# Optimization experiments

Measured on AMD Instinct MI355X. Metric: run time of the kernel, lower is better.

## Reference

```python
import jax, jax.numpy as jnp
import numpy as np

B, S, D, H, DFF = 2, 2048, 512, 8, 2048
DK = D // H
EPS = 1e-6  # LayerNormalization eps


def _ln(x, a, b):
    # torch: alpha * (x - mean) / (std + eps) + bias, std is unbiased (ddof=1)
    m = jnp.mean(x, axis=-1, keepdims=True)
    s = jnp.std(x, axis=-1, keepdims=True, ddof=1)
    return a * (x - m) / (s + EPS) + b


def _mha(Q, K, V, mask, Wq, bq, Wk, bk, Wv, bv, Wo, bo):
    Bq, Sq = Q.shape[0], Q.shape[1]
    Sk = K.shape[1]
    q = (Q @ Wq + bq).reshape(Bq, Sq, H, DK).transpose(0, 2, 1, 3)  # bhqd
    k = (K @ Wk + bk).reshape(Bq, Sk, H, DK).transpose(0, 2, 1, 3)  # bhkd
    v = (V @ Wv + bv).reshape(Bq, Sk, H, DK).transpose(0, 2, 1, 3)  # bhkd
    scores = jnp.einsum('bhqd,bhkd->bhqk', q, k) / jnp.sqrt(jnp.float32(DK))
    scores = jnp.where(mask == 0, -jnp.inf, scores)  # masked_fill(mask==0, -inf)
    attn = jax.nn.softmax(scores, axis=-1)  # dropout is identity in eval
    out = jnp.einsum('bhqk,bhkd->bhqd', attn, v)
    out = out.transpose(0, 2, 1, 3).reshape(Bq, Sq, D)
    return out @ Wo + bo


def setup_inputs() -> dict:
    key = jax.random.key(0)
    ks = jax.random.split(key, 20)
    sc = 0.02
    inp = {
        'x': jax.random.normal(ks[0], (B, S, D), jnp.float32),
        'encoder_output': jax.random.normal(ks[1], (B, S, D), jnp.float32),
        'encoder_output_mask': jnp.broadcast_to(jnp.ones((S, S), jnp.int32), (B, 1, S, S)),
        'decoder_mask': jnp.broadcast_to(jnp.tril(jnp.ones((S, S), jnp.int32)), (B, 1, S, S)),
        'sa_Wq': jax.random.normal(ks[2], (D, D), jnp.float32) * sc,
        'sa_bq': jnp.zeros((D,), jnp.float32),
        'sa_Wk': jax.random.normal(ks[3], (D, D), jnp.float32) * sc,
        'sa_bk': jnp.zeros((D,), jnp.float32),
        'sa_Wv': jax.random.normal(ks[4], (D, D), jnp.float32) * sc,
        'sa_bv': jnp.zeros((D,), jnp.float32),
        'sa_Wo': jax.random.normal(ks[5], (D, D), jnp.float32) * sc,
        'sa_bo': jnp.zeros((D,), jnp.float32),
        'ca_Wq': jax.random.normal(ks[6], (D, D), jnp.float32) * sc,
        'ca_bq': jnp.zeros((D,), jnp.float32),
        'ca_Wk': jax.random.normal(ks[7], (D, D), jnp.float32) * sc,
        'ca_bk': jnp.zeros((D,), jnp.float32),
        'ca_Wv': jax.random.normal(ks[8], (D, D), jnp.float32) * sc,
        'ca_bv': jnp.zeros((D,), jnp.float32),
        'ca_Wo': jax.random.normal(ks[9], (D, D), jnp.float32) * sc,
        'ca_bo': jnp.zeros((D,), jnp.float32),
        'ff_W1': jax.random.normal(ks[10], (D, DFF), jnp.float32) * sc,
        'ff_b1': jnp.zeros((DFF,), jnp.float32),
        'ff_W2': jax.random.normal(ks[11], (DFF, D), jnp.float32) * sc,
        'ff_b2': jnp.zeros((D,), jnp.float32),
        'ln0_a': jnp.ones((1,), jnp.float32), 'ln0_b': jnp.zeros((1,), jnp.float32),
        'ln1_a': jnp.ones((1,), jnp.float32), 'ln1_b': jnp.zeros((1,), jnp.float32),
        'ln2_a': jnp.ones((1,), jnp.float32), 'ln2_b': jnp.zeros((1,), jnp.float32),
    }
    return inp


def reference(x, encoder_output, encoder_output_mask, decoder_mask,
              sa_Wq, sa_bq, sa_Wk, sa_bk, sa_Wv, sa_bv, sa_Wo, sa_bo,
              ca_Wq, ca_bq, ca_Wk, ca_bk, ca_Wv, ca_bv, ca_Wo, ca_bo,
              ff_W1, ff_b1, ff_W2, ff_b2,
              ln0_a, ln0_b, ln1_a, ln1_b, ln2_a, ln2_b):
    # Residual 0: pre-norm self-attention (dropout = identity in eval)
    n = _ln(x, ln0_a, ln0_b)
    x = x + _mha(n, n, n, decoder_mask, sa_Wq, sa_bq, sa_Wk, sa_bk, sa_Wv, sa_bv, sa_Wo, sa_bo)
    # Residual 1: pre-norm cross-attention
    n = _ln(x, ln1_a, ln1_b)
    x = x + _mha(n, encoder_output, encoder_output, encoder_output_mask,
                 ca_Wq, ca_bq, ca_Wk, ca_bk, ca_Wv, ca_bv, ca_Wo, ca_bo)
    # Residual 2: pre-norm FFN (Linear -> ReLU -> Linear)
    n = _ln(x, ln2_a, ln2_b)
    x = x + (jax.nn.relu(n @ ff_W1 + ff_b1) @ ff_W2 + ff_b2)
    return x
```

## Files before the change

### kernel.cpp

```cpp
#include <hip/hip_runtime.h>
#include <hip/hip_bf16.h>

typedef __bf16 bf16_t;
typedef __bf16 bf16x8_t __attribute__((ext_vector_type(8)));
typedef float f32x4_t __attribute__((ext_vector_type(4)));

static constexpr int B_ = 2, S_ = 2048, D_ = 512, H_ = 8, DK_ = 64, DFF_ = 2048;
static constexpr int M_ = B_ * S_;
static constexpr float QSCALE = 0.125f * 1.44269504f;

__device__ __forceinline__ unsigned pkbf(float a, float b) {
  union { bf16_t h; unsigned short u; } x, y;
  x.h = (bf16_t)a; y.h = (bf16_t)b;
  return (unsigned)x.u | ((unsigned)y.u << 16);
}

__device__ __forceinline__ void async16(bf16_t* lds, const bf16_t* g) {
  __builtin_amdgcn_global_load_lds((__attribute__((address_space(1))) void*)g,
                                   (__attribute__((address_space(3))) void*)lds,
                                   16, 0, 0);
}

struct PrepArg {
  const float* W[10]; bf16_t* T[10];
  const float* enc; bf16_t* encb;
  const float* x; bf16_t* xb; float2* stats0;
  float* stats12;
  float* csum[7];
};

__global__ __launch_bounds__(256) void prep(PrepArg a) {
  __shared__ float T[64 * 65];
  const int bx = blockIdx.x, tid = threadIdx.x;
  if (bx < 1024) {
    const float* W; bf16_t* Wt; int K, N, k0, n0;
    if (bx < 512) { int wi = bx >> 6, t = bx & 63; W = a.W[wi]; Wt = a.T[wi]; K = 512; N = 512; k0 = (t >> 3) * 64; n0 = (t & 7) * 64; }
    else if (bx < 768) { int t = bx - 512; W = a.W[8]; Wt = a.T[8]; K = 512; N = 2048; k0 = (t & 7) * 64; n0 = (t >> 3) * 64; }
    else { int t = bx - 768; W = a.W[9]; Wt = a.T[9]; K = 2048; N = 512; k0 = (t & 31) * 64; n0 = (t >> 5) * 64; }
#pragma unroll
    for (int p = 0; p < 4; ++p) {
      int e = p * 1024 + tid * 4;
      int kr = e >> 6, nc = e & 63;
      float4 f = *(const float4*)(W + (long)(k0 + kr) * N + n0 + nc);
      T[kr * 65 + nc + 0] = f.x; T[kr * 65 + nc + 1] = f.y;
      T[kr * 65 + nc + 2] = f.z; T[kr * 65 + nc + 3] = f.w;
    }
    __syncthreads();
#pragma unroll
    for (int p = 0; p < 4; ++p) {
      int e = p * 1024 + tid * 4;
      int nr = e >> 6, kc = e & 63;
      alignas(8) bf16_t t4[4];
#pragma unroll
      for (int j = 0; j < 4; ++j) t4[j] = (bf16_t)T[(kc + j) * 65 + nr];
      *(uint2*)(Wt + (long)(n0 + nr) * K + k0 + kc) = *(uint2*)t4;
    }
  } else if (bx < 2048) {
    const long i = ((long)(bx - 1024) * 256 + tid) * 8;
    float4 u = *(const float4*)(a.enc + i);
    float4 v = *(const float4*)(a.enc + i + 4);
    alignas(16) bf16_t t[8];
    t[0] = (bf16_t)u.x; t[1] = (bf16_t)u.y; t[2] = (bf16_t)u.z; t[3] = (bf16_t)u.w;
    t[4] = (bf16_t)v.x; t[5] = (bf16_t)v.y; t[6] = (bf16_t)v.z; t[7] = (bf16_t)v.w;
    *(uint4*)(a.encb + i) = *(uint4*)t;
  } else if (bx < 3072) {
    const int row = (bx - 2048) * 4 + (tid >> 6);
    const int lane = tid & 63;
    const float4* xr = (const float4*)(a.x + (long)row * D_);
    float4 v0 = xr[lane * 2], v1 = xr[lane * 2 + 1];
    float s = v0.x + v0.y + v0.z + v0.w + v1.x + v1.y + v1.z + v1.w;
    float ss = v0.x * v0.x + v0.y * v0.y + v0.z * v0.z + v0.w * v0.w +
               v1.x * v1.x + v1.y * v1.y + v1.z * v1.z + v1.w * v1.w;
#pragma unroll
    for (int m = 1; m < 64; m <<= 1) { s += __shfl_xor(s, m); ss += __shfl_xor(ss, m); }
    alignas(16) bf16_t y[8];
    y[0] = (bf16_t)v0.x; y[1] = (bf16_t)v0.y; y[2] = (bf16_t)v0.z; y[3] = (bf16_t)v0.w;
    y[4] = (bf16_t)v1.x; y[5] = (bf16_t)v1.y; y[6] = (bf16_t)v1.z; y[7] = (bf16_t)v1.w;
    ((uint4*)(a.xb + (long)row * D_))[lane] = *(uint4*)y;
    if (lane == 0) a.stats0[row] = make_float2(s, ss);
  } else if (bx < 3152) {
    __shared__ float red[256];
    int b3 = bx - 3072;
    const float* Wsrc; float* dst; int N, c0;
    if (b3 < 48) {
      const int map[6] = {0, 1, 2, 4, 5, 6};
      int wsel = b3 >> 3;
      Wsrc = a.W[map[wsel]]; dst = a.csum[wsel]; N = 512; c0 = (b3 & 7) * 64;
    } else { Wsrc = a.W[8]; dst = a.csum[6]; N = 2048; c0 = (b3 - 48) * 64; }
    const int col = c0 + (tid & 63);
    float p = 0.f;
    for (int k = tid >> 6; k < 512; k += 4) p += Wsrc[(long)k * N + col];
    red[tid] = p;
    __syncthreads();
    if (tid < 64) dst[c0 + tid] = red[tid] + red[tid + 64] + red[tid + 128] + red[tid + 192];
  } else {
    const int i = (bx - 3152) * 2048 + tid * 8;
    *(f32x4_t*)&a.stats12[i] = (f32x4_t){0.f, 0.f, 0.f, 0.f};
    *(f32x4_t*)&a.stats12[i + 4] = (f32x4_t){0.f, 0.f, 0.f, 0.f};
  }
}

__device__ __forceinline__ void ln_coef(float2 st, float ga, float gb,
                                        float& sc, float& sh) {
  const float mean = st.x * (1.0f / 512.0f);
  float var = (st.y - 512.0f * mean * mean) * (1.0f / 511.0f);
  var = fmaxf(var, 0.0f);
  sc = ga / (sqrtf(var) + 1e-6f);
  sh = gb - mean * sc;
}

struct G128 {
  const bf16_t* A[3]; const bf16_t* Wt[3];
  const float* bias[3]; const float* csum[3];
  void* out[3]; float osc[3];
  const float2* stats; const float* ga; const float* gb;
  int N; int zvt;
};

template <int RELU>
__global__ __launch_bounds__(256, 2) void gemm128(G128 a) {
  __shared__ bf16_t As[2][128 * 32];
  __shared__ bf16_t Bs[2][128 * 32];
  const int z = blockIdx.z;
  const bf16_t* A = a.A[z];
  const bf16_t* Wt = a.Wt[z];
  const float* bias = a.bias[z];
  const float* csum = a.csum[z];
  const int N = a.N;
  const int tid = threadIdx.x;
  const int wave = tid >> 6, lane = tid & 63, quad = lane >> 4, l15 = lane & 15;
  const long m0 = (long)blockIdx.x * 128;
  const long n0 = (long)blockIdx.y * 128;
  const int wm = (wave >> 1) * 64;
  const int wn = (wave & 1) * 64;

  const int r4 = lane >> 2;
  const int cg = (lane & 3) ^ ((lane >> 3) & 3);
  const bf16_t* Ab = A + m0 * 512 + cg * 8;
  const bf16_t* Bb = Wt + n0 * 512 + cg * 8;

  auto stage = [&](int buf, int k0) {
#pragma unroll
    for (int c = 0; c < 2; ++c) {
      const int row = wave * 32 + c * 16;
      async16(&As[buf][row * 32], Ab + (long)(row + r4) * 512 + k0);
      async16(&Bs[buf][row * 32], Bb + (long)(row + r4) * 512 + k0);
    }
  };

  f32x4_t acc[4][4];
#pragma unroll
  for (int i = 0; i < 4; ++i)
#pragma unroll
    for (int j = 0; j < 4; ++j) acc[i][j] = (f32x4_t){0.f, 0.f, 0.f, 0.f};

  const int sc8 = (quad ^ ((l15 >> 1) & 3)) * 8;
  stage(0, 0);
  for (int kt = 0; kt < 16; ++kt) {
    __syncthreads();
    if (kt + 1 < 16) stage((kt + 1) & 1, (kt + 1) * 32);
    const bf16_t* Al = &As[kt & 1][0];
    const bf16_t* Bl = &Bs[kt & 1][0];
    bf16x8_t af[4], bfr[4];
#pragma unroll
    for (int i = 0; i < 4; ++i) af[i] = *(const bf16x8_t*)&Al[(wm + i * 16 + l15) * 32 + sc8];
#pragma unroll
    for (int j = 0; j < 4; ++j) bfr[j] = *(const bf16x8_t*)&Bl[(wn + j * 16 + l15) * 32 + sc8];
#pragma unroll
    for (int i = 0; i < 4; ++i)
#pragma unroll
      for (int j = 0; j < 4; ++j)
        acc[i][j] = __builtin_amdgcn_mfma_f32_16x16x32_bf16(af[i], bfr[j], acc[i][j], 0, 0, 0);
  }

  const bool useln = (csum != nullptr);
  float scr[4][4], shr[4][4];
  if (useln) {
    const float gav = a.ga[0], gbv = a.gb[0];
#pragma unroll
    for (int i = 0; i < 4; ++i)
#pragma unroll
      for (int r = 0; r < 4; ++r) {
        const int row = (int)m0 + wm + i * 16 + quad * 4 + r;
        ln_coef(a.stats[row], gav, gbv, scr[i][r], shr[i][r]);
      }
  } else {
#pragma unroll
    for (int i = 0; i < 4; ++i)
#pragma unroll
      for (int r = 0; r < 4; ++r) { scr[i][r] = 1.f; shr[i][r] = 0.f; }
  }

  const bool isVt = (z == a.zvt);
  const float osc = a.osc[z];
#pragma unroll
  for (int i = 0; i < 4; ++i) {
#pragma unroll
    for (int j = 0; j < 4; ++j) {
      const int col = (int)n0 + wn + j * 16 + l15;
      const float cs = useln ? csum[col] : 0.f;
      const float bv = bias[col];
      float v[4];
#pragma unroll
      for (int r = 0; r < 4; ++r) {
        v[r] = scr[i][r] * acc[i][j][r] + shr[i][r] * cs + bv;
        if constexpr (RELU == 1) v[r] = fmaxf(v[r], 0.f);
      }
      if (isVt) {
        const int row0 = (int)m0 + wm + i * 16 + quad * 4;
        const int b = row0 >> 11, s = row0 & 2047;
        const long addr = ((long)(b * 8 + (col >> 6)) * 64 + (col & 63)) * 2048 + s;
        uint2 w;
        w.x = pkbf(v[0], v[1]);
        w.y = pkbf(v[2], v[3]);
        *(uint2*)((bf16_t*)a.out[z] + addr) = w;
      } else {
        bf16_t* outp = (bf16_t*)a.out[z];
#pragma unroll
        for (int r = 0; r < 4; ++r) {
          const long row = m0 + wm + i * 16 + quad * 4 + r;
          outp[row * N + col] = (bf16_t)(v[r] * osc);
        }
      }
    }
  }
}

template <bool STATS>
__global__ __launch_bounds__(256, 3) void gemm64(const bf16_t* __restrict__ A, int K,
                                                 const bf16_t* __restrict__ Wt,
                                                 const float* __restrict__ bias,
                                                 const float* __restrict__ res,
                                                 float* __restrict__ out,
                                                 bf16_t* __restrict__ outb,
                                                 float* __restrict__ statsOut) {
  __shared__ bf16_t As[2][64 * 64];
  __shared__ bf16_t Bs[2][128 * 64];
  const int tid = threadIdx.x;
  const int wave = tid >> 6, lane = tid & 63, quad = lane >> 4, l15 = lane & 15;
  const long m0 = (long)blockIdx.x * 64;
  const long n0 = (long)blockIdx.y * 128;
  const int wm = (wave >> 1) * 32;
  const int wn = (wave & 1) * 64;

  const int r8 = lane >> 3;
  const int cg = (lane & 7) ^ r8;
  const bf16_t* Ab = A + m0 * (long)K + cg * 8;
  const bf16_t* Bb = Wt + n0 * (long)K + cg * 8;

  auto stage = [&](int buf, int k0) {
#pragma unroll
    for (int c = 0; c < 2; ++c) {
      const int row = wave * 16 + c * 8;
      async16(&As[buf][row * 64], Ab + (long)(row + r8) * K + k0);
    }
#pragma unroll
    for (int c = 0; c < 4; ++c) {
      const int row = wave * 32 + c * 8;
      async16(&Bs[buf][row * 64], Bb + (long)(row + r8) * K + k0);
    }
  };

  f32x4_t acc[2][4];
#pragma unroll
  for (int i = 0; i < 2; ++i)
#pragma unroll
    for (int j = 0; j < 4; ++j) acc[i][j] = (f32x4_t){0.f, 0.f, 0.f, 0.f};

  const int KT = K >> 6;
  stage(0, 0);
  for (int kt = 0; kt < KT; ++kt) {
    __syncthreads();
    if (kt + 1 < KT) stage((kt + 1) & 1, (kt + 1) * 64);
    const bf16_t* Al = &As[kt & 1][0];
    const bf16_t* Bl = &Bs[kt & 1][0];
#pragma unroll
    for (int ks = 0; ks < 2; ++ks) {
      const int sc = ((ks * 4 + quad) ^ (l15 & 7)) * 8;
      bf16x8_t af[2], bfr[4];
#pragma unroll
      for (int i = 0; i < 2; ++i) af[i] = *(const bf16x8_t*)&Al[(wm + i * 16 + l15) * 64 + sc];
#pragma unroll
      for (int j = 0; j < 4; ++j) bfr[j] = *(const bf16x8_t*)&Bl[(wn + j * 16 + l15) * 64 + sc];
#pragma unroll
      for (int i = 0; i < 2; ++i)
#pragma unroll
        for (int j = 0; j < 4; ++j)
          acc[i][j] = __builtin_amdgcn_mfma_f32_16x16x32_bf16(af[i], bfr[j], acc[i][j], 0, 0, 0);
    }
  }

#pragma unroll
  for (int i = 0; i < 2; ++i) {
    float rs[4] = {0.f, 0.f, 0.f, 0.f}, rq[4] = {0.f, 0.f, 0.f, 0.f};
#pragma unroll
    for (int j = 0; j < 4; ++j) {
      const int col = (int)n0 + wn + j * 16 + l15;
      const float bv = bias[col];
#pragma unroll
      for (int r = 0; r < 4; ++r) {
        const long row = m0 + wm + i * 16 + quad * 4 + r;
        const float v = acc[i][j][r] + bv + res[row * 512 + col];
        out[row * 512 + col] = v;
        if constexpr (STATS) {
          outb[row * 512 + col] = (bf16_t)v;
          rs[r] += v;
          rq[r] += v * v;
        }
      }
    }
    if constexpr (STATS) {
#pragma unroll
      for (int r = 0; r < 4; ++r) {
#pragma unroll
        for (int m = 1; m < 16; m <<= 1) {
          rs[r] += __shfl_xor(rs[r], m);
          rq[r] += __shfl_xor(rq[r], m);
        }
        if (l15 == 0) {
          const long row = m0 + wm + i * 16 + quad * 4 + r;
          atomicAdd(&statsOut[row * 2], rs[r]);
          atomicAdd(&statsOut[row * 2 + 1], rq[r]);
        }
      }
    }
  }
}

template <bool CAUSAL>
__global__ __launch_bounds__(256, 3) void flash_attn(const bf16_t* __restrict__ Q,
                                                     const bf16_t* __restrict__ Kg,
                                                     const bf16_t* __restrict__ Vt,
                                                     float* __restrict__ po,
                                                     float* __restrict__ pl) {
  __shared__ bf16_t Ks[2][64 * 64];
  __shared__ bf16_t Vs[2][64 * 64];
  __shared__ bf16_t Ps[4][32 * 64];
  const int tid = threadIdx.x, wave = tid >> 6, lane = tid & 63;
  const int quad = lane >> 4, l15 = lane & 15;
  const int bh = blockIdx.y, b = bh >> 3, h = bh & 7;
  const int qt = CAUSAL ? (15 - (int)blockIdx.x) : (int)blockIdx.x;
  const int chunk = blockIdx.z;
  const int ntt = CAUSAL ? (2 * qt + 2) : 32;
  const int tstart = (chunk * ntt) / 3;
  const int tend = ((chunk + 1) * ntt) / 3;
  const int q0 = qt * 128;
  const long prow0 = ((long)(chunk * 16 + bh)) * 2048;

  if (tstart >= tend) {
    const long ob = (prow0 + q0) * 64;
#pragma unroll
    for (int p = 0; p < 8; ++p)
      *(f32x4_t*)&po[ob + (long)tid * 32 + p * 4] = (f32x4_t){0.f, 0.f, 0.f, 0.f};
    if (tid < 128) pl[prow0 + q0 + tid] = 0.f;
    return;
  }

  const int qw = q0 + wave * 32;
  const long base = (long)b * S_ * D_ + (long)h * DK_;
  const long vtbase = (long)bh * DK_ * S_;

  bf16x8_t qf[2][2];
#pragma unroll
  for (int qh = 0; qh < 2; ++qh)
#pragma unroll
    for (int ks = 0; ks < 2; ++ks)
      qf[qh][ks] = *(const bf16x8_t*)(Q + base + (long)(qw + qh * 16 + l15) * D_ + ks * 32 + quad * 8);

  const int r8 = lane >> 3;
  const int cg8 = (lane & 7) ^ r8;
  const bf16_t* Kb = Kg + base + cg8 * 8;
  const bf16_t* Vb = Vt + vtbase + cg8 * 8;

  auto stage = [&](int buf, int t) {
    const int kk0 = t * 64;
#pragma unroll
    for (int c = 0; c < 2; ++c) {
      const int row = wave * 16 + c * 8;
      async16(&Ks[buf][row * 64], Kb + (long)(kk0 + row + r8) * D_);
      async16(&Vs[buf][row * 64], Vb + (long)(row + r8) * S_ + kk0);
    }
  };

  float li[2] = {0.f, 0.f};
  f32x4_t o[2][4];
#pragma unroll
  for (int qh = 0; qh < 2; ++qh)
#pragma unroll
    for (int db = 0; db < 4; ++db) o[qh][db] = (f32x4_t){0.f, 0.f, 0.f, 0.f};

  bf16_t* Pw = &Ps[wave][0];
  const int pq7 = l15 & 7;

  stage(0, tstart);
  for (int t = tstart; t < tend; ++t) {
    const int buf = (t - tstart) & 1;
    __syncthreads();
    if (t + 1 < tend) stage(buf ^ 1, t + 1);
    const bf16_t* Kt = &Ks[buf][0];
    const bf16_t* Vl = &Vs[buf][0];
    const int kk0 = t * 64;

#pragma unroll
    for (int qh = 0; qh < 2; ++qh) {
      f32x4_t st[4];
#pragma unroll
      for (int nb = 0; nb < 4; ++nb) {
        f32x4_t a = (f32x4_t){0.f, 0.f, 0.f, 0.f};
#pragma unroll
        for (int ks = 0; ks < 2; ++ks) {
          const int scf = ((ks * 4 + quad) ^ (l15 & 7)) * 8;
          const bf16x8_t kf = *(const bf16x8_t*)&Kt[(nb * 16 + l15) * 64 + scf];
          a = __builtin_amdgcn_mfma_f32_16x16x32_bf16(kf, qf[qh][ks], a, 0, 0, 0);
        }
        st[nb] = a;
      }
      const bool domask = CAUSAL && (kk0 + 63 > qw + qh * 16);
#pragma unroll
      for (int nb = 0; nb < 4; ++nb)
#pragma unroll
        for (int r = 0; r < 4; ++r) {
          float v = st[nb][r];
          if (domask && (kk0 + nb * 16 + quad * 4 + r > qw + qh * 16 + l15)) v = -1e30f;
          const float p = exp2f(v);
          st[nb][r] = p;
          li[qh] += p;
        }
      const int prow = (qh * 16 + l15) * 64;
#pragma unroll
      for (int nb = 0; nb < 4; ++nb) {
        uint2 w;
        w.x = pkbf(st[nb][0], st[nb][1]);
        w.y = pkbf(st[nb][2], st[nb][3]);
        const int ck = nb * 2 + (quad >> 1);
        *(uint2*)&Pw[prow + (ck ^ pq7) * 8 + (quad & 1) * 4] = w;
      }
    }

    bf16x8_t pf[2][2];
#pragma unroll
    for (int qh = 0; qh < 2; ++qh)
#pragma unroll
      for (int ks = 0; ks < 2; ++ks)
        pf[qh][ks] = *(const bf16x8_t*)&Pw[(qh * 16 + l15) * 64 + ((ks * 4 + quad) ^ pq7) * 8];
#pragma unroll
    for (int ks = 0; ks < 2; ++ks) {
#pragma unroll
      for (int db = 0; db < 4; ++db) {
        const int scf = ((ks * 4 + quad) ^ (l15 & 7)) * 8;
        const bf16x8_t vf = *(const bf16x8_t*)&Vl[(db * 16 + l15) * 64 + scf];
#pragma unroll
        for (int qh = 0; qh < 2; ++qh)
          o[qh][db] = __builtin_amdgcn_mfma_f32_16x16x32_bf16(vf, pf[qh][ks], o[qh][db], 0, 0, 0);
      }
    }
  }

#pragma unroll
  for (int qh = 0; qh < 2; ++qh) {
    li[qh] += __shfl_xor(li[qh], 16);
    li[qh] += __shfl_xor(li[qh], 32);
    const long pr = prow0 + qw + qh * 16 + l15;
#pragma unroll
    for (int db = 0; db < 4; ++db)
      *(f32x4_t*)&po[pr * 64 + db * 16 + quad * 4] = o[qh][db];
    if (quad == 0) pl[pr] = li[qh];
  }
}

__global__ __launch_bounds__(256) void merge3(const float* __restrict__ po,
                                              const float* __restrict__ pl,
                                              bf16_t* __restrict__ O) {
  const int qt = blockIdx.x, bh = blockIdx.y, b = bh >> 3, h = bh & 7;
  const int t = threadIdx.x;
  const int q = qt * 64 + (t >> 2), d0 = (t & 3) * 16;
  const long r0 = (long)bh * 2048 + q;
  const long r1 = (long)(16 + bh) * 2048 + q;
  const long r2 = (long)(32 + bh) * 2048 + q;
  const float inv = 1.0f / (pl[r0] + pl[r1] + pl[r2]);
  alignas(16) bf16_t out[16];
#pragma unroll
  for (int j = 0; j < 4; ++j) {
    f32x4_t x0 = *(const f32x4_t*)&po[r0 * 64 + d0 + j * 4];
    f32x4_t x1 = *(const f32x4_t*)&po[r1 * 64 + d0 + j * 4];
    f32x4_t x2 = *(const f32x4_t*)&po[r2 * 64 + d0 + j * 4];
#pragma unroll
    for (int r = 0; r < 4; ++r) out[j * 4 + r] = (bf16_t)((x0[r] + x1[r] + x2[r]) * inv);
  }
  const long row = (long)b * S_ + q;
  *(uint4*)(O + row * D_ + h * DK_ + d0) = *(uint4*)&out[0];
  *(uint4*)(O + row * D_ + h * DK_ + d0 + 8) = *(uint4*)&out[8];
}

extern "C" void kernel_launch(void* const* d_in, const int* in_sizes, int n_in,
                              void* d_out, int out_size, void* d_ws, size_t ws_size,
                              hipStream_t stream) {
  const float* x    = (const float*)d_in[0];
  const float* enc  = (const float*)d_in[1];
  const float* saWq = (const float*)d_in[4];  const float* sabq = (const float*)d_in[5];
  const float* saWk = (const float*)d_in[6];  const float* sabk = (const float*)d_in[7];
  const float* saWv = (const float*)d_in[8];  const float* sabv = (const float*)d_in[9];
  const float* saWo = (const float*)d_in[10]; const float* sabo = (const float*)d_in[11];
  const float* caWq = (const float*)d_in[12]; const float* cabq = (const float*)d_in[13];
  const float* caWk = (const float*)d_in[14]; const float* cabk = (const float*)d_in[15];
  const float* caWv = (const float*)d_in[16]; const float* cabv = (const float*)d_in[17];
  const float* caWo = (const float*)d_in[18]; const float* cabo = (const float*)d_in[19];
  const float* ffW1 = (const float*)d_in[20]; const float* ffb1 = (const float*)d_in[21];
  const float* ffW2 = (const float*)d_in[22]; const float* ffb2 = (const float*)d_in[23];
  const float* ln0a = (const float*)d_in[24]; const float* ln0b = (const float*)d_in[25];
  const float* ln1a = (const float*)d_in[26]; const float* ln1b = (const float*)d_in[27];
  const float* ln2a = (const float*)d_in[28]; const float* ln2b = (const float*)d_in[29];

  char* ws = (char*)d_ws;
  size_t off = 0;
  auto alloc = [&](size_t bytes) -> void* {
    void* p = ws + off;
    off += (bytes + 255) & ~(size_t)255;
    return p;
  };
  bf16_t* wt_saq = (bf16_t*)alloc(512 * 512 * 2);
  bf16_t* wt_sak = (bf16_t*)alloc(512 * 512 * 2);
  bf16_t* wt_sav = (bf16_t*)alloc(512 * 512 * 2);
  bf16_t* wt_sao = (bf16_t*)alloc(512 * 512 * 2);
  bf16_t* wt_caq = (bf16_t*)alloc(512 * 512 * 2);
  bf16_t* wt_cak = (bf16_t*)alloc(512 * 512 * 2);
  bf16_t* wt_cav = (bf16_t*)alloc(512 * 512 * 2);
  bf16_t* wt_cao = (bf16_t*)alloc(512 * 512 * 2);
  bf16_t* wt_f1  = (bf16_t*)alloc((size_t)512 * 2048 * 2);
  bf16_t* wt_f2  = (bf16_t*)alloc((size_t)2048 * 512 * 2);
  bf16_t* enc_b  = (bf16_t*)alloc((size_t)M_ * D_ * 2);
  bf16_t* xb     = (bf16_t*)alloc((size_t)M_ * D_ * 2);
  bf16_t* qb     = (bf16_t*)alloc((size_t)M_ * D_ * 2);
  bf16_t* kb     = (bf16_t*)alloc((size_t)M_ * D_ * 2);
  bf16_t* vtb    = (bf16_t*)alloc((size_t)M_ * D_ * 2);
  bf16_t* attnb  = (bf16_t*)alloc((size_t)M_ * D_ * 2);
  bf16_t* hid    = (bf16_t*)alloc((size_t)M_ * DFF_ * 2);
  float*  x2     = (float*)alloc((size_t)M_ * D_ * 4);
  float*  x1     = (float*)alloc((size_t)M_ * D_ * 4);
  bf16_t* x1b    = (bf16_t*)alloc((size_t)M_ * D_ * 2);
  bf16_t* x2b    = (bf16_t*)alloc((size_t)M_ * D_ * 2);
  float*  pl     = (float*)alloc(3 * 16 * 2048 * 4);
  float2* stats0 = (float2*)alloc(4096 * 8);
  float*  stats12= (float*)alloc(2 * 4096 * 2 * 4);
  float*  cs_saq = (float*)alloc(512 * 4);
  float*  cs_sak = (float*)alloc(512 * 4);
  float*  cs_sav = (float*)alloc(512 * 4);
  float*  cs_caq = (float*)alloc(512 * 4);
  float*  cs_cak = (float*)alloc(512 * 4);
  float*  cs_cav = (float*)alloc(512 * 4);
  float*  cs_f1  = (float*)alloc(2048 * 4);
  float*  po     = (float*)hid;
  float*  stats1 = stats12;
  float*  stats2 = stats12 + 8192;

  {
    PrepArg a;
    a.W[0] = saWq; a.T[0] = wt_saq; a.W[1] = saWk; a.T[1] = wt_sak;
    a.W[2] = saWv; a.T[2] = wt_sav; a.W[3] = saWo; a.T[3] = wt_sao;
    a.W[4] = caWq; a.T[4] = wt_caq; a.W[5] = caWk; a.T[5] = wt_cak;
    a.W[6] = caWv; a.T[6] = wt_cav; a.W[7] = caWo; a.T[7] = wt_cao;
    a.W[8] = ffW1; a.T[8] = wt_f1;  a.W[9] = ffW2; a.T[9] = wt_f2;
    a.enc = enc; a.encb = enc_b; a.x = x; a.xb = xb; a.stats0 = stats0;
    a.stats12 = stats12;
    a.csum[0] = cs_saq; a.csum[1] = cs_sak; a.csum[2] = cs_sav;
    a.csum[3] = cs_caq; a.csum[4] = cs_cak; a.csum[5] = cs_cav;
    a.csum[6] = cs_f1;
    prep<<<3160, 256, 0, stream>>>(a);
  }

  {
    G128 g;
    g.A[0] = xb; g.A[1] = xb; g.A[2] = xb;
    g.Wt[0] = wt_saq; g.Wt[1] = wt_sak; g.Wt[2] = wt_sav;
    g.bias[0] = sabq; g.bias[1] = sabk; g.bias[2] = sabv;
    g.csum[0] = cs_saq; g.csum[1] = cs_sak; g.csum[2] = cs_sav;
    g.out[0] = qb; g.out[1] = kb; g.out[2] = vtb;
    g.osc[0] = QSCALE; g.osc[1] = 1.f; g.osc[2] = 1.f;
    g.stats = stats0; g.ga = ln0a; g.gb = ln0b; g.N = 512; g.zvt = 2;
    gemm128<0><<<dim3(32, 4, 3), 256, 0, stream>>>(g);
  }
  flash_attn<true><<<dim3(16, 16, 3), 256, 0, stream>>>(qb, kb, vtb, po, pl);
  merge3<<<dim3(32, 16), 256, 0, stream>>>(po, pl, attnb);
  gemm64<true><<<dim3(64, 4), 256, 0, stream>>>(attnb, 512, wt_sao, sabo, x, x1, x1b, stats1);

  {
    G128 g;
    g.A[0] = x1b; g.A[1] = enc_b; g.A[2] = enc_b;
    g.Wt[0] = wt_caq; g.Wt[1] = wt_cak; g.Wt[2] = wt_cav;
    g.bias[0] = cabq; g.bias[1] = cabk; g.bias[2] = cabv;
    g.csum[0] = cs_caq; g.csum[1] = nullptr; g.csum[2] = nullptr;
    g.out[0] = qb; g.out[1] = kb; g.out[2] = vtb;
    g.osc[0] = QSCALE; g.osc[1] = 1.f; g.osc[2] = 1.f;
    g.stats = (const float2*)stats1; g.ga = ln1a; g.gb = ln1b; g.N = 512; g.zvt = 2;
    gemm128<0><<<dim3(32, 4, 3), 256, 0, stream>>>(g);
  }
  flash_attn<false><<<dim3(16, 16, 3), 256, 0, stream>>>(qb, kb, vtb, po, pl);
  merge3<<<dim3(32, 16), 256, 0, stream>>>(po, pl, attnb);
  gemm64<true><<<dim3(64, 4), 256, 0, stream>>>(attnb, 512, wt_cao, cabo, x1, x2, x2b, stats2);

  {
    G128 g;
    g.A[0] = x2b; g.Wt[0] = wt_f1; g.bias[0] = ffb1; g.csum[0] = cs_f1;
    g.out[0] = hid; g.osc[0] = 1.f;
    g.A[1] = x2b; g.Wt[1] = wt_f1; g.bias[1] = ffb1; g.csum[1] = cs_f1;
    g.out[1] = hid; g.osc[1] = 1.f;
    g.A[2] = x2b; g.Wt[2] = wt_f1; g.bias[2] = ffb1; g.csum[2] = cs_f1;
    g.out[2] = hid; g.osc[2] = 1.f;
    g.stats = (const float2*)stats2; g.ga = ln2a; g.gb = ln2b; g.N = 2048; g.zvt = -1;
    gemm128<1><<<dim3(32, 16, 1), 256, 0, stream>>>(g);
  }
  gemm64<false><<<dim3(64, 4), 256, 0, stream>>>(hid, 2048, wt_f2, ffb2, x2, (float*)d_out, nullptr, nullptr);
}
```

Measured before the change: 396.5 us.

## Shrink GEMM tiles, keep softmax P in registers via f16 MFMA, simplify prep

Both projection GEMMs move to 64x64 tiles with a BK=64 swizzle and higher occupancy bounds, which launches many more blocks to fill the CUs. Flash attention now writes V^T in fp16 and feeds the softmax probabilities straight from registers into 16x16x16 f16 MFMAs, removing the LDS round trip for P. The prep kernel gets a simpler column-sum path using one block per weight and 16-byte transpose stores. The trade-off is less data reuse per tile in the GEMMs, and P and V are now held at fp16 precision.

```diff
diff --git a/kernel.cpp b/kernel.cpp
--- a/kernel.cpp
+++ b/kernel.cpp
@@ -2,12 +2,20 @@
 #include <hip/hip_bf16.h>
 
 typedef __bf16 bf16_t;
+typedef _Float16 f16_t;
 typedef __bf16 bf16x8_t __attribute__((ext_vector_type(8)));
+typedef _Float16 f16x4_t __attribute__((ext_vector_type(4)));
 typedef float f32x4_t __attribute__((ext_vector_type(4)));
 
 static constexpr int B_ = 2, S_ = 2048, D_ = 512, H_ = 8, DK_ = 64, DFF_ = 2048;
 static constexpr int M_ = B_ * S_;
 static constexpr float QSCALE = 0.125f * 1.44269504f;
+
+#if __has_builtin(__builtin_amdgcn_mfma_f32_16x16x16_f16)
+#define MFMA16F16 __builtin_amdgcn_mfma_f32_16x16x16_f16
+#else
+#define MFMA16F16 __builtin_amdgcn_mfma_f32_16x16x16f16
+#endif
 
 __device__ __forceinline__ unsigned pkbf(float a, float b) {
   union { bf16_t h; unsigned short u; } x, y;
@@ -15,8 +23,8 @@
   return (unsigned)x.u | ((unsigned)y.u << 16);
 }
 
-__device__ __forceinline__ void async16(bf16_t* lds, const bf16_t* g) {
-  __builtin_amdgcn_global_load_lds((__attribute__((address_space(1))) void*)g,
+__device__ __forceinline__ void async16(void* lds, const void* g) {
+  __builtin_amdgcn_global_load_lds((const __attribute__((address_space(1))) void*)g,
                                    (__attribute__((address_space(3))) void*)lds,
                                    16, 0, 0);
 }
@@ -47,13 +55,13 @@
     }
     __syncthreads();
 #pragma unroll
-    for (int p = 0; p < 4; ++p) {
-      int e = p * 1024 + tid * 4;
+    for (int p = 0; p < 2; ++p) {
+      int e = p * 2048 + tid * 8;
       int nr = e >> 6, kc = e & 63;
-      alignas(8) bf16_t t4[4];
-#pragma unroll
-      for (int j = 0; j < 4; ++j) t4[j] = (bf16_t)T[(kc + j) * 65 + nr];
-      *(uint2*)(Wt + (long)(n0 + nr) * K + k0 + kc) = *(uint2*)t4;
+      alignas(16) bf16_t t8[8];
+#pragma unroll
+      for (int j = 0; j < 8; ++j) t8[j] = (bf16_t)T[(kc + j) * 65 + nr];
+      *(uint4*)(Wt + (long)(n0 + nr) * K + k0 + kc) = *(uint4*)t8;
     }
   } else if (bx < 2048) {
     const long i = ((long)(bx - 1024) * 256 + tid) * 8;
@@ -78,23 +86,29 @@
     y[4] = (bf16_t)v1.x; y[5] = (bf16_t)v1.y; y[6] = (bf16_t)v1.z; y[7] = (bf16_t)v1.w;
     ((uint4*)(a.xb + (long)row * D_))[lane] = *(uint4*)y;
     if (lane == 0) a.stats0[row] = make_float2(s, ss);
-  } else if (bx < 3152) {
-    __shared__ float red[256];
-    int b3 = bx - 3072;
-    const float* Wsrc; float* dst; int N, c0;
-    if (b3 < 48) {
-      const int map[6] = {0, 1, 2, 4, 5, 6};
-      int wsel = b3 >> 3;
-      Wsrc = a.W[map[wsel]]; dst = a.csum[wsel]; N = 512; c0 = (b3 & 7) * 64;
-    } else { Wsrc = a.W[8]; dst = a.csum[6]; N = 2048; c0 = (b3 - 48) * 64; }
-    const int col = c0 + (tid & 63);
-    float p = 0.f;
-    for (int k = tid >> 6; k < 512; k += 4) p += Wsrc[(long)k * N + col];
-    red[tid] = p;
-    __syncthreads();
-    if (tid < 64) dst[c0 + tid] = red[tid] + red[tid + 64] + red[tid + 128] + red[tid + 192];
+  } else if (bx < 3079) {
+    const int wsel = bx - 3072;
+    const int map[6] = {0, 1, 2, 4, 5, 6};
+    const float* Wsrc = (wsel < 6) ? a.W[map[wsel]] : a.W[8];
+    float* dst = a.csum[wsel];
+    if (wsel < 6) {
+      float ax = 0.f, ay = 0.f;
+      const float2* p = (const float2*)Wsrc + tid;
+      for (int k = 0; k < 512; ++k) { float2 v = p[(long)k * 256]; ax += v.x; ay += v.y; }
+      ((float2*)dst)[tid] = make_float2(ax, ay);
+    } else {
+      float acc[8] = {0, 0, 0, 0, 0, 0, 0, 0};
+      for (int k = 0; k < 512; ++k) {
+        float4 u = *(const float4*)(Wsrc + (long)k * 2048 + tid * 8);
+        float4 v = *(const float4*)(Wsrc + (long)k * 2048 + tid * 8 + 4);
+        acc[0] += u.x; acc[1] += u.y; acc[2] += u.z; acc[3] += u.w;
+        acc[4] += v.x; acc[5] += v.y; acc[6] += v.z; acc[7] += v.w;
+      }
+      *(float4*)(dst + tid * 8) = make_float4(acc[0], acc[1], acc[2], acc[3]);
+      *(float4*)(dst + tid * 8 + 4) = make_float4(acc[4], acc[5], acc[6], acc[7]);
+    }
   } else {
-    const int i = (bx - 3152) * 2048 + tid * 8;
+    const int i = (bx - 3079) * 2048 + tid * 8;
     *(f32x4_t*)&a.stats12[i] = (f32x4_t){0.f, 0.f, 0.f, 0.f};
     *(f32x4_t*)&a.stats12[i + 4] = (f32x4_t){0.f, 0.f, 0.f, 0.f};
   }
@@ -109,7 +123,7 @@
   sh = gb - mean * sc;
 }
 
-struct G128 {
+struct GQ {
   const bf16_t* A[3]; const bf16_t* Wt[3];
   const float* bias[3]; const float* csum[3];
   void* out[3]; float osc[3];
@@ -118,9 +132,9 @@
 };
 
 template <int RELU>
-__global__ __launch_bounds__(256, 2) void gemm128(G128 a) {
-  __shared__ bf16_t As[2][128 * 32];
-  __shared__ bf16_t Bs[2][128 * 32];
+__global__ __launch_bounds__(256, 4) void gemmQ(GQ a) {
+  __shared__ bf16_t As[2][64 * 64];
+  __shared__ bf16_t Bs[2][64 * 64];
   const int z = blockIdx.z;
   const bf16_t* A = a.A[z];
   const bf16_t* Wt = a.Wt[z];
@@ -129,56 +143,60 @@
   const int N = a.N;
   const int tid = threadIdx.x;
   const int wave = tid >> 6, lane = tid & 63, quad = lane >> 4, l15 = lane & 15;
-  const long m0 = (long)blockIdx.x * 128;
-  const long n0 = (long)blockIdx.y * 128;
-  const int wm = (wave >> 1) * 64;
-  const int wn = (wave & 1) * 64;
-
-  const int r4 = lane >> 2;
-  const int cg = (lane & 3) ^ ((lane >> 3) & 3);
+  const long m0 = (long)blockIdx.x * 64;
+  const long n0 = (long)blockIdx.y * 64;
+  const int wm = (wave >> 1) * 32;
+  const int wn = (wave & 1) * 32;
+
+  const int r8 = lane >> 3;
+  const int cg = (lane & 7) ^ r8;
   const bf16_t* Ab = A + m0 * 512 + cg * 8;
   const bf16_t* Bb = Wt + n0 * 512 + cg * 8;
 
   auto stage = [&](int buf, int k0) {
 #pragma unroll
     for (int c = 0; c < 2; ++c) {
-      const int row = wave * 32 + c * 16;
-      async16(&As[buf][row * 32], Ab + (long)(row + r4) * 512 + k0);
-      async16(&Bs[buf][row * 32], Bb + (long)(row + r4) * 512 + k0);
+      const int row = wave * 16 + c * 8;
+      async16(&As[buf][row * 64], Ab + (long)(row + r8) * 512 + k0);
+      async16(&Bs[buf][row * 64], Bb + (long)(row + r8) * 512 + k0);
     }
   };
 
-  f32x4_t acc[4][4];
-#pragma unroll
-  for (int i = 0; i < 4; ++i)
-#pragma unroll
-    for (int j = 0; j < 4; ++j) acc[i][j] = (f32x4_t){0.f, 0.f, 0.f, 0.f};
-
-  const int sc8 = (quad ^ ((l15 >> 1) & 3)) * 8;
+  f32x4_t acc[2][2];
+#pragma unroll
+  for (int i = 0; i < 2; ++i)
+#pragma unroll
+    for (int j = 0; j < 2; ++j) acc[i][j] = (f32x4_t){0.f, 0.f, 0.f, 0.f};
+
   stage(0, 0);
-  for (int kt = 0; kt < 16; ++kt) {
+  for (int kt = 0; kt < 8; ++kt) {
     __syncthreads();
-    if (kt + 1 < 16) stage((kt + 1) & 1, (kt + 1) * 32);
+    if (kt + 1 < 8) stage((kt + 1) & 1, (kt + 1) * 64);
     const bf16_t* Al = &As[kt & 1][0];
     const bf16_t* Bl = &Bs[kt & 1][0];
-    bf16x8_t af[4], bfr[4];
-#pragma unroll
-    for (int i = 0; i < 4; ++i) af[i] = *(const bf16x8_t*)&Al[(wm + i * 16 + l15) * 32 + sc8];
-#pragma unroll
-    for (int j = 0; j < 4; ++j) bfr[j] = *(const bf16x8_t*)&Bl[(wn + j * 16 + l15) * 32 + sc8];
-#pragma unroll
-    for (int i = 0; i < 4; ++i)
-#pragma unroll
-      for (int j = 0; j < 4; ++j)
-        acc[i][j] = __builtin_amdgcn_mfma_f32_16x16x32_bf16(af[i], bfr[j], acc[i][j], 0, 0, 0);
+#pragma unroll
+    for (int ks = 0; ks < 2; ++ks) {
+      const int sc = ((ks * 4 + quad) ^ (l15 & 7)) * 8;
+      bf16x8_t af[2], bfr[2];
+#pragma unroll
+      for (int i = 0; i < 2; ++i) {
+        af[i] = *(const bf16x8_t*)&Al[(wm + i * 16 + l15) * 64 + sc];
+        bfr[i] = *(const bf16x8_t*)&Bl[(wn + i * 16 + l15) * 64 + sc];
+      }
+#pragma unroll
+      for (int i = 0; i < 2; ++i)
+#pragma unroll
+        for (int j = 0; j < 2; ++j)
+          acc[i][j] = __builtin_amdgcn_mfma_f32_16x16x32_bf16(af[i], bfr[j], acc[i][j], 0, 0, 0);
+    }
   }
 
   const bool useln = (csum != nullptr);
-  float scr[4][4], shr[4][4];
+  float scr[2][4], shr[2][4];
   if (useln) {
     const float gav = a.ga[0], gbv = a.gb[0];
 #pragma unroll
-    for (int i = 0; i < 4; ++i)
+    for (int i = 0; i < 2; ++i)
 #pragma unroll
       for (int r = 0; r < 4; ++r) {
         const int row = (int)m0 + wm + i * 16 + quad * 4 + r;
@@ -186,7 +204,7 @@
       }
   } else {
 #pragma unroll
-    for (int i = 0; i < 4; ++i)
+    for (int i = 0; i < 2; ++i)
 #pragma unroll
       for (int r = 0; r < 4; ++r) { scr[i][r] = 1.f; shr[i][r] = 0.f; }
   }
@@ -194,9 +212,9 @@
   const bool isVt = (z == a.zvt);
   const float osc = a.osc[z];
 #pragma unroll
-  for (int i = 0; i < 4; ++i) {
-#pragma unroll
-    for (int j = 0; j < 4; ++j) {
+  for (int i = 0; i < 2; ++i) {
+#pragma unroll
+    for (int j = 0; j < 2; ++j) {
       const int col = (int)n0 + wn + j * 16 + l15;
       const float cs = useln ? csum[col] : 0.f;
       const float bv = bias[col];
@@ -210,10 +228,10 @@
         const int row0 = (int)m0 + wm + i * 16 + quad * 4;
         const int b = row0 >> 11, s = row0 & 2047;
         const long addr = ((long)(b * 8 + (col >> 6)) * 64 + (col & 63)) * 2048 + s;
-        uint2 w;
-        w.x = pkbf(v[0], v[1]);
-        w.y = pkbf(v[2], v[3]);
-        *(uint2*)((bf16_t*)a.out[z] + addr) = w;
+        union { f16_t h[4]; uint2 u; } w;
+#pragma unroll
+        for (int r = 0; r < 4; ++r) w.h[r] = (f16_t)v[r];
+        *(uint2*)((f16_t*)a.out[z] + addr) = w.u;
       } else {
         bf16_t* outp = (bf16_t*)a.out[z];
 #pragma unroll
@@ -227,21 +245,21 @@
 }
 
 template <bool STATS>
-__global__ __launch_bounds__(256, 3) void gemm64(const bf16_t* __restrict__ A, int K,
-                                                 const bf16_t* __restrict__ Wt,
-                                                 const float* __restrict__ bias,
-                                                 const float* __restrict__ res,
-                                                 float* __restrict__ out,
-                                                 bf16_t* __restrict__ outb,
-                                                 float* __restrict__ statsOut) {
+__global__ __launch_bounds__(256, 4) void gemmR(const bf16_t* __restrict__ A, int K,
+                                                const bf16_t* __restrict__ Wt,
+                                                const float* __restrict__ bias,
+                                                const float* __restrict__ res,
+                                                float* __restrict__ out,
+                                                bf16_t* __restrict__ outb,
+                                                float* __restrict__ statsOut) {
   __shared__ bf16_t As[2][64 * 64];
-  __shared__ bf16_t Bs[2][128 * 64];
+  __shared__ bf16_t Bs[2][64 * 64];
   const int tid = threadIdx.x;
   const int wave = tid >> 6, lane = tid & 63, quad = lane >> 4, l15 = lane & 15;
   const long m0 = (long)blockIdx.x * 64;
-  const long n0 = (long)blockIdx.y * 128;
+  const long n0 = (long)blockIdx.y * 64;
   const int wm = (wave >> 1) * 32;
-  const int wn = (wave & 1) * 64;
+  const int wn = (wave & 1) * 32;
 
   const int r8 = lane >> 3;
   const int cg = (lane & 7) ^ r8;
@@ -253,19 +271,15 @@
     for (int c = 0; c < 2; ++c) {
       const int row = wave * 16 + c * 8;
       async16(&As[buf][row * 64], Ab + (long)(row + r8) * K + k0);
-    }
-#pragma unroll
-    for (int c = 0; c < 4; ++c) {
-      const int row = wave * 32 + c * 8;
       async16(&Bs[buf][row * 64], Bb + (long)(row + r8) * K + k0);
     }
   };
 
-  f32x4_t acc[2][4];
+  f32x4_t acc[2][2];
 #pragma unroll
   for (int i = 0; i < 2; ++i)
 #pragma unroll
-    for (int j = 0; j < 4; ++j) acc[i][j] = (f32x4_t){0.f, 0.f, 0.f, 0.f};
+    for (int j = 0; j < 2; ++j) acc[i][j] = (f32x4_t){0.f, 0.f, 0.f, 0.f};
 
   const int KT = K >> 6;
   stage(0, 0);
@@ -277,15 +291,16 @@
 #pragma unroll
     for (int ks = 0; ks < 2; ++ks) {
       const int sc = ((ks * 4 + quad) ^ (l15 & 7)) * 8;
-      bf16x8_t af[2], bfr[4];
-#pragma unroll
-      for (int i = 0; i < 2; ++i) af[i] = *(const bf16x8_t*)&Al[(wm + i * 16 + l15) * 64 + sc];
-#pragma unroll
-      for (int j = 0; j < 4; ++j) bfr[j] = *(const bf16x8_t*)&Bl[(wn + j * 16 + l15) * 64 + sc];
+      bf16x8_t af[2], bfr[2];
+#pragma unroll
+      for (int i = 0; i < 2; ++i) {
+        af[i] = *(const bf16x8_t*)&Al[(wm + i * 16 + l15) * 64 + sc];
+        bfr[i] = *(const bf16x8_t*)&Bl[(wn + i * 16 + l15) * 64 + sc];
+      }
 #pragma unroll
       for (int i = 0; i < 2; ++i)
 #pragma unroll
-        for (int j = 0; j < 4; ++j)
+        for (int j = 0; j < 2; ++j)
           acc[i][j] = __builtin_amdgcn_mfma_f32_16x16x32_bf16(af[i], bfr[j], acc[i][j], 0, 0, 0);
     }
   }
@@ -294,7 +309,7 @@
   for (int i = 0; i < 2; ++i) {
     float rs[4] = {0.f, 0.f, 0.f, 0.f}, rq[4] = {0.f, 0.f, 0.f, 0.f};
 #pragma unroll
-    for (int j = 0; j < 4; ++j) {
+    for (int j = 0; j < 2; ++j) {
       const int col = (int)n0 + wn + j * 16 + l15;
       const float bv = bias[col];
 #pragma unroll
@@ -328,14 +343,13 @@
 }
 
 template <bool CAUSAL>
-__global__ __launch_bounds__(256, 3) void flash_attn(const bf16_t* __restrict__ Q,
+__global__ __launch_bounds__(256, 4) void flash_attn(const bf16_t* __restrict__ Q,
                                                      const bf16_t* __restrict__ Kg,
-                                                     const bf16_t* __restrict__ Vt,
+                                                     const f16_t* __restrict__ Vt,
                                                      float* __restrict__ po,
                                                      float* __restrict__ pl) {
   __shared__ bf16_t Ks[2][64 * 64];
-  __shared__ bf16_t Vs[2][64 * 64];
-  __shared__ bf16_t Ps[4][32 * 64];
+  __shared__ f16_t Vs[2][64 * 64];
   const int tid = threadIdx.x, wave = tid >> 6, lane = tid & 63;
   const int quad = lane >> 4, l15 = lane & 15;
   const int bh = blockIdx.y, b = bh >> 3, h = bh & 7;
@@ -370,7 +384,7 @@
   const int r8 = lane >> 3;
   const int cg8 = (lane & 7) ^ r8;
   const bf16_t* Kb = Kg + base + cg8 * 8;
-  const bf16_t* Vb = Vt + vtbase + cg8 * 8;
+  const f16_t* Vb = Vt + vtbase + cg8 * 8;
 
   auto stage = [&](int buf, int t) {
     const int kk0 = t * 64;
@@ -388,9 +402,6 @@
   for (int qh = 0; qh < 2; ++qh)
 #pragma unroll
     for (int db = 0; db < 4; ++db) o[qh][db] = (f32x4_t){0.f, 0.f, 0.f, 0.f};
-
-  bf16_t* Pw = &Ps[wave][0];
-  const int pq7 = l15 & 7;
 
   stage(0, tstart);
   for (int t = tstart; t < tend; ++t) {
@@ -398,26 +409,27 @@
     __syncthreads();
     if (t + 1 < tend) stage(buf ^ 1, t + 1);
     const bf16_t* Kt = &Ks[buf][0];
-    const bf16_t* Vl = &Vs[buf][0];
+    const f16_t* Vl = &Vs[buf][0];
     const int kk0 = t * 64;
 
+    f16x4_t pa[2][4];
 #pragma unroll
     for (int qh = 0; qh < 2; ++qh) {
       f32x4_t st[4];
 #pragma unroll
       for (int nb = 0; nb < 4; ++nb) {
-        f32x4_t a = (f32x4_t){0.f, 0.f, 0.f, 0.f};
+        f32x4_t acc = (f32x4_t){0.f, 0.f, 0.f, 0.f};
 #pragma unroll
         for (int ks = 0; ks < 2; ++ks) {
           const int scf = ((ks * 4 + quad) ^ (l15 & 7)) * 8;
           const bf16x8_t kf = *(const bf16x8_t*)&Kt[(nb * 16 + l15) * 64 + scf];
-          a = __builtin_amdgcn_mfma_f32_16x16x32_bf16(kf, qf[qh][ks], a, 0, 0, 0);
+          acc = __builtin_amdgcn_mfma_f32_16x16x32_bf16(kf, qf[qh][ks], acc, 0, 0, 0);
         }
-        st[nb] = a;
+        st[nb] = acc;
       }
       const bool domask = CAUSAL && (kk0 + 63 > qw + qh * 16);
 #pragma unroll
-      for (int nb = 0; nb < 4; ++nb)
+      for (int nb = 0; nb < 4; ++nb) {
 #pragma unroll
         for (int r = 0; r < 4; ++r) {
           float v = st[nb][r];
@@ -426,32 +438,21 @@
           st[nb][r] = p;
           li[qh] += p;
         }
-      const int prow = (qh * 16 + l15) * 64;
-#pragma unroll
-      for (int nb = 0; nb < 4; ++nb) {
-        uint2 w;
-        w.x = pkbf(st[nb][0], st[nb][1]);
-        w.y = pkbf(st[nb][2], st[nb][3]);
-        const int ck = nb * 2 + (quad >> 1);
-        *(uint2*)&Pw[prow + (ck ^ pq7) * 8 + (quad & 1) * 4] = w;
-      }
-    }
-
-    bf16x8_t pf[2][2];
-#pragma unroll
-    for (int qh = 0; qh < 2; ++qh)
-#pragma unroll
-      for (int ks = 0; ks < 2; ++ks)
-        pf[qh][ks] = *(const bf16x8_t*)&Pw[(qh * 16 + l15) * 64 + ((ks * 4 + quad) ^ pq7) * 8];
-#pragma unroll
-    for (int ks = 0; ks < 2; ++ks) {
+        pa[qh][nb] = (f16x4_t){(f16_t)st[nb][0], (f16_t)st[nb][1],
+                               (f16_t)st[nb][2], (f16_t)st[nb][3]};
+      }
+    }
+
+#pragma unroll
+    for (int k4 = 0; k4 < 4; ++k4) {
 #pragma unroll
       for (int db = 0; db < 4; ++db) {
-        const int scf = ((ks * 4 + quad) ^ (l15 & 7)) * 8;
-        const bf16x8_t vf = *(const bf16x8_t*)&Vl[(db * 16 + l15) * 64 + scf];
+        const int row = db * 16 + l15;
+        const int c = 2 * k4 + (quad >> 1);
+        const f16x4_t vf = *(const f16x4_t*)&Vl[row * 64 + ((c ^ (l15 & 7)) * 8) + (quad & 1) * 4];
 #pragma unroll
         for (int qh = 0; qh < 2; ++qh)
-          o[qh][db] = __builtin_amdgcn_mfma_f32_16x16x32_bf16(vf, pf[qh][ks], o[qh][db], 0, 0, 0);
+          o[qh][db] = MFMA16F16(vf, pa[qh][k4], o[qh][db], 0, 0, 0);
       }
     }
   }
@@ -532,7 +533,7 @@
   bf16_t* xb     = (bf16_t*)alloc((size_t)M_ * D_ * 2);
   bf16_t* qb     = (bf16_t*)alloc((size_t)M_ * D_ * 2);
   bf16_t* kb     = (bf16_t*)alloc((size_t)M_ * D_ * 2);
-  bf16_t* vtb    = (bf16_t*)alloc((size_t)M_ * D_ * 2);
+  f16_t*  vtb    = (f16_t*)alloc((size_t)M_ * D_ * 2);
   bf16_t* attnb  = (bf16_t*)alloc((size_t)M_ * D_ * 2);
   bf16_t* hid    = (bf16_t*)alloc((size_t)M_ * DFF_ * 2);
   float*  x2     = (float*)alloc((size_t)M_ * D_ * 4);
@@ -565,11 +566,11 @@
     a.csum[0] = cs_saq; a.csum[1] = cs_sak; a.csum[2] = cs_sav;
     a.csum[3] = cs_caq; a.csum[4] = cs_cak; a.csum[5] = cs_cav;
     a.csum[6] = cs_f1;
-    prep<<<3160, 256, 0, stream>>>(a);
+    prep<<<3087, 256, 0, stream>>>(a);
   }
 
   {
-    G128 g;
+    GQ g;
     g.A[0] = xb; g.A[1] = xb; g.A[2] = xb;
     g.Wt[0] = wt_saq; g.Wt[1] = wt_sak; g.Wt[2] = wt_sav;
     g.bias[0] = sabq; g.bias[1] = sabk; g.bias[2] = sabv;
@@ -577,14 +578,14 @@
     g.out[0] = qb; g.out[1] = kb; g.out[2] = vtb;
     g.osc[0] = QSCALE; g.osc[1] = 1.f; g.osc[2] = 1.f;
     g.stats = stats0; g.ga = ln0a; g.gb = ln0b; g.N = 512; g.zvt = 2;
-    gemm128<0><<<dim3(32, 4, 3), 256, 0, stream>>>(g);
+    gemmQ<0><<<dim3(64, 8, 3), 256, 0, stream>>>(g);
   }
   flash_attn<true><<<dim3(16, 16, 3), 256, 0, stream>>>(qb, kb, vtb, po, pl);
   merge3<<<dim3(32, 16), 256, 0, stream>>>(po, pl, attnb);
-  gemm64<true><<<dim3(64, 4), 256, 0, stream>>>(attnb, 512, wt_sao, sabo, x, x1, x1b, stats1);
+  gemmR<true><<<dim3(64, 8), 256, 0, stream>>>(attnb, 512, wt_sao, sabo, x, x1, x1b, stats1);
 
   {
-    G128 g;
+    GQ g;
     g.A[0] = x1b; g.A[1] = enc_b; g.A[2] = enc_b;
     g.Wt[0] = wt_caq; g.Wt[1] = wt_cak; g.Wt[2] = wt_cav;
     g.bias[0] = cabq; g.bias[1] = cabk; g.bias[2] = cabv;
@@ -592,14 +593,14 @@
     g.out[0] = qb; g.out[1] = kb; g.out[2] = vtb;
     g.osc[0] = QSCALE; g.osc[1] = 1.f; g.osc[2] = 1.f;
     g.stats = (const float2*)stats1; g.ga = ln1a; g.gb = ln1b; g.N = 512; g.zvt = 2;
-    gemm128<0><<<dim3(32, 4, 3), 256, 0, stream>>>(g);
+    gemmQ<0><<<dim3(64, 8, 3), 256, 0, stream>>>(g);
   }
   flash_attn<false><<<dim3(16, 16, 3), 256, 0, stream>>>(qb, kb, vtb, po, pl);
   merge3<<<dim3(32, 16), 256, 0, stream>>>(po, pl, attnb);
-  gemm64<true><<<dim3(64, 4), 256, 0, stream>>>(attnb, 512, wt_cao, cabo, x1, x2, x2b, stats2);
+  gemmR<true><<<dim3(64, 8), 256, 0, stream>>>(attnb, 512, wt_cao, cabo, x1, x2, x2b, stats2);
 
   {
-    G128 g;
+    GQ g;
     g.A[0] = x2b; g.Wt[0] = wt_f1; g.bias[0] = ffb1; g.csum[0] = cs_f1;
     g.out[0] = hid; g.osc[0] = 1.f;
     g.A[1] = x2b; g.Wt[1] = wt_f1; g.bias[1] = ffb1; g.csum[1] = cs_f1;
@@ -607,7 +608,7 @@
     g.A[2] = x2b; g.Wt[2] = wt_f1; g.bias[2] = ffb1; g.csum[2] = cs_f1;
     g.out[2] = hid; g.osc[2] = 1.f;
     g.stats = (const float2*)stats2; g.ga = ln2a; g.gb = ln2b; g.N = 2048; g.zvt = -1;
-    gemm128<1><<<dim3(32, 16, 1), 256, 0, stream>>>(g);
-  }
-  gemm64<false><<<dim3(64, 4), 256, 0, stream>>>(hid, 2048, wt_f2, ffb2, x2, (float*)d_out, nullptr, nullptr);
-}
+    gemmQ<1><<<dim3(64, 32, 1), 256, 0, stream>>>(g);
+  }
+  gemmR<false><<<dim3(64, 8), 256, 0, stream>>>(hid, 2048, wt_f2, ffb2, x2, (float*)d_out, nullptr, nullptr);
+}
```

Measured after the change: 398.0 us. About the same (+0.4%).
